# Optimization experiments

Measured on AMD Instinct MI355X. Metric: run time of the kernel, lower is better.

The kernel has to match this reference:

```python
import jax, jax.numpy as jnp
import numpy as np

D = 256          # input_dim (node embedding dim)
ATT_TIMES = 2
ATT_NUM = 2
DIN = D * ATT_NUM  # NTN input dim = 512
F = 16           # feature_map_dim


def setup_inputs() -> dict:
    key = jax.random.key(0)
    ks = jax.random.split(key, 10)
    x1 = jax.random.normal(ks[0], (120000, D), dtype=jnp.float32)
    x2 = jax.random.normal(ks[1], (100000, D), dtype=jnp.float32)
    # attention weight (glorot)
    W0 = jax.random.normal(ks[2], (D, D), dtype=jnp.float32) * (2.0 / (D + D)) ** 0.5
    # NTN params
    V = jax.random.normal(ks[3], (F, 2 * DIN), dtype=jnp.float32) * (2.0 / (F + 2 * DIN)) ** 0.5
    W = jax.random.normal(ks[4], (F, DIN, DIN), dtype=jnp.float32) * (2.0 / (DIN + DIN)) ** 0.5
    b = jax.random.normal(ks[5], (F,), dtype=jnp.float32)
    # projection MLP 16->8->4->2->1, torch Linear weights are (out, in)
    P0 = jax.random.normal(ks[6], (8, 16), dtype=jnp.float32) * (2.0 / (8 + 16)) ** 0.5
    P1 = jax.random.normal(ks[7], (4, 8), dtype=jnp.float32) * (2.0 / (4 + 8)) ** 0.5
    P2 = jax.random.normal(ks[8], (2, 4), dtype=jnp.float32) * (2.0 / (2 + 4)) ** 0.5
    P3 = jax.random.normal(ks[9], (1, 2), dtype=jnp.float32) * (2.0 / (1 + 2)) ** 0.5
    return {"x1": x1, "x2": x2, "W0": W0, "V": V, "W": W, "b": b,
            "P0": P0, "P1": P1, "P2": P2, "P3": P3}


def _attention(x, W0):
    # x: (N, D) -> (1, D*ATT_NUM) graph embedding.
    outs = []
    for _ in range(ATT_NUM):  # 'dot' style: same params each head (eye W), kept for faithfulness
        cur = x
        out = None
        for _ in range(ATT_TIMES):
            temp = jnp.mean(cur, axis=0, keepdims=True)          # (1, D)
            h_avg = jnp.tanh(temp @ W0)                          # att_weight=True
            att = jax.nn.sigmoid(cur @ h_avg.T)                  # (N, 1), W=eye in 'dot' style
            out = att.T @ cur                                    # (1, D)
            cur = cur * att
        outs.append(out)
    return jnp.concatenate(outs, axis=1)                         # (1, DIN)


def _ntn(g1, g2, V, W, b):
    # g1, g2: (1, DIN). Fused bilinear over all F feature maps.
    concat = jnp.concatenate([g1, g2], axis=1)                   # (1, 2*DIN)
    v_term = concat @ V.T                                        # (1, F)
    w_term = jnp.einsum('nd,fde,me->nf', g1, W, g2)              # (1, F)
    return jax.nn.sigmoid(v_term + w_term + b)                   # inneract = sigmoid


def reference(x1, x2, W0, V, W, b, P0, P1, P2, P3):
    g1 = _attention(x1, W0)
    g2 = _attention(x2, W0)
    x = _ntn(g1, g2, V, W, b)                                    # (1, F), branch 'an'
    for P in (P0, P1, P2, P3):                                   # Linear(no bias) + Sigmoid
        x = jax.nn.sigmoid(x @ P.T)
    return x                                                     # (1, 1)
```

## Files before the change

kernel.cpp:

```cpp
#include <hip/hip_runtime.h>
#include <math.h>

#define DD 256
#define REPS 8

#define OFF_SUMREP 0
#define OFF_H1P    4096
#define OFF_S1REP  4608
#define OFF_H2P    8704
#define OFF_OREP   9216
#define OFF_WTREP  13824
#define WS_FLOATS  13952
#define MIRROR_OFF_BYTES 65536

typedef float    f32x4 __attribute__((ext_vector_type(4)));
typedef float    f32x8 __attribute__((ext_vector_type(8)));
typedef _Float16 f16x4 __attribute__((ext_vector_type(4)));
typedef _Float16 f16x8 __attribute__((ext_vector_type(8)));

__device__ __forceinline__ float sigmoidf_(float x) { return 1.0f / (1.0f + __expf(-x)); }

__device__ __forceinline__ f32x8 ld8(const f16x8* p, size_t i) {
    return __builtin_convertvector(p[i], f32x8);
}
__device__ __forceinline__ f32x8 ld8(const f32x8* p, size_t i) { return p[i]; }

__device__ __forceinline__ float dot8(f32x8 a, f32x8 b) {
    f32x8 m = a * b;
    return ((m[0] + m[4]) + (m[1] + m[5])) + ((m[2] + m[6]) + (m[3] + m[7]));
}

__global__ void k_zero(float* __restrict__ ws) {
    int i = blockIdx.x * 256 + threadIdx.x;
    if (i < WS_FLOATS) ws[i] = 0.0f;
}

__device__ __forceinline__ void block_reduce_atomic4(f32x4 acc, int t, float* dst_base) {
    __shared__ f32x4 lds[256];
    lds[t] = acc;
    __syncthreads();
    if (t < 64) {
        f32x4 s = lds[t] + lds[t + 64] + lds[t + 128] + lds[t + 192];
        float* dst = dst_base + t * 4;
        atomicAdd(dst + 0, s.x); atomicAdd(dst + 1, s.y);
        atomicAdd(dst + 2, s.z); atomicAdd(dst + 3, s.w);
    }
}

__device__ __forceinline__ void block_reduce_atomic8(f32x8 acc, int t, float* dst_base) {
    __shared__ f32x8 lds8[256];
    lds8[t] = acc;
    __syncthreads();
    const float* lf = (const float*)lds8;
    float s = 0.f;
#pragma unroll
    for (int slot = 0; slot < 8; slot++) s += lf[slot * 256 + t];
    atomicAdd(dst_base + t, s);
}

template<bool WM>
__global__ void k_mean_t(const f32x4* __restrict__ x1, const f32x4* __restrict__ x2,
                         f16x4* __restrict__ m1, f16x4* __restrict__ m2,
                         int N1, int N2, float* __restrict__ ws) {
    int b = blockIdx.x, t = threadIdx.x;
    int inp = (b < 512) ? 0 : 1;
    int bl = inp ? (b - 512) : b;
    const f32x4* x = inp ? x2 : x1;
    f16x4* mm = inp ? m2 : m1;
    int N = inp ? N2 : N1;
    int col4 = t & 63, rg = t >> 6;
    f32x4 acc = {0.f, 0.f, 0.f, 0.f};
    for (int r = bl * 4 + rg; r < N; r += 2048) {
        size_t i0 = (size_t)r * 64 + col4;
        f32x4 v = __builtin_nontemporal_load(&x[i0]);
        if (WM) mm[i0] = __builtin_convertvector(v, f16x4);
        acc += v;
    }
    block_reduce_atomic4(acc, t, ws + OFF_SUMREP + inp * (REPS * 256) + (bl & (REPS - 1)) * 256);
}

__global__ void k_hpart(const float* __restrict__ W0, float* __restrict__ ws,
                        int srcOff, int dstOff, int N1, int N2) {
    int inp = blockIdx.x >> 4, g = blockIdx.x & 15;
    int t = threadIdx.x;
    __shared__ float temp[16];
    if (t < 16) {
        const float* src = ws + srcOff + inp * (REPS * 256) + g * 16 + t;
        float s = 0.f;
#pragma unroll
        for (int r = 0; r < REPS; r++) s += src[r * 256];
        temp[t] = s * (1.0f / (float)(inp ? N2 : N1));
    }
    __syncthreads();
    float p = 0.f;
#pragma unroll
    for (int j = 0; j < 16; j++) p += temp[j] * W0[(g * 16 + j) * 256 + t];
    atomicAdd(ws + dstOff + inp * 256 + t, p);
}

template<typename T>
__global__ void k_att1_t(const T* __restrict__ b1, const T* __restrict__ b2,
                         int N1, int N2, float* __restrict__ ws) {
    int b = blockIdx.x, t = threadIdx.x;
    int inp = (b < 512) ? 0 : 1;
    int bl = inp ? (b - 512) : b;
    const T* x = inp ? b2 : b1;
    int N = inp ? N2 : N1;
    int lane = t & 63, w = t >> 6;
    int half = lane >> 5, l32 = lane & 31;
    f32x8 h1;
#pragma unroll
    for (int j = 0; j < 8; j++) h1[j] = tanhf(ws[OFF_H1P + inp * 256 + l32 * 8 + j]);
    f32x8 acc = {0.f, 0.f, 0.f, 0.f, 0.f, 0.f, 0.f, 0.f};
    int wid = bl * 4 + w;
    int base = wid * 2;
    for (; base + 1 < N; base += 4096) {
        int row = base + half;
        f32x8 v = ld8(x, (size_t)row * 32 + l32);
        float d = dot8(v, h1);
#pragma unroll
        for (int off = 16; off; off >>= 1) d += __shfl_xor(d, off, 64);
        acc += sigmoidf_(d) * v;
    }
    if (base < N && half == 0) {
        f32x8 v = ld8(x, (size_t)base * 32 + l32);
        float d = dot8(v, h1);
#pragma unroll
        for (int off = 16; off; off >>= 1) d += __shfl_xor(d, off, 64);
        acc += sigmoidf_(d) * v;
    }
    block_reduce_atomic8(acc, t, ws + OFF_S1REP + inp * (REPS * 256) + (bl & (REPS - 1)) * 256);
}

template<typename T>
__global__ void k_att2_t(const T* __restrict__ b1, const T* __restrict__ b2,
                         int N1, int N2, float* __restrict__ ws) {
    int b = blockIdx.x, t = threadIdx.x;
    int inp = (b < 512) ? 0 : 1;
    int bl = inp ? (b - 512) : b;
    const T* x = inp ? b2 : b1;
    int N = inp ? N2 : N1;
    int lane = t & 63, w = t >> 6;
    int half = lane >> 5, l32 = lane & 31;
    f32x8 h1, h2;
#pragma unroll
    for (int j = 0; j < 8; j++) {
        h1[j] = tanhf(ws[OFF_H1P + inp * 256 + l32 * 8 + j]);
        h2[j] = tanhf(ws[OFF_H2P + inp * 256 + l32 * 8 + j]);
    }
    f32x8 acc = {0.f, 0.f, 0.f, 0.f, 0.f, 0.f, 0.f, 0.f};
    int wid = bl * 4 + w;
    int base = wid * 2;
    for (; base + 1 < N; base += 4096) {
        int row = base + half;
        f32x8 v = ld8(x, (size_t)row * 32 + l32);
        float d = dot8(v, h1), e = dot8(v, h2);
#pragma unroll
        for (int off = 16; off; off >>= 1) {
            d += __shfl_xor(d, off, 64); e += __shfl_xor(e, off, 64);
        }
        float a1 = sigmoidf_(d);
        acc += (a1 * sigmoidf_(a1 * e)) * v;
    }
    if (base < N && half == 0) {
        f32x8 v = ld8(x, (size_t)base * 32 + l32);
        float d = dot8(v, h1), e = dot8(v, h2);
#pragma unroll
        for (int off = 16; off; off >>= 1) {
            d += __shfl_xor(d, off, 64); e += __shfl_xor(e, off, 64);
        }
        float a1 = sigmoidf_(d);
        acc += (a1 * sigmoidf_(a1 * e)) * v;
    }
    block_reduce_atomic8(acc, t, ws + OFF_OREP + inp * (REPS * 256) + (bl & (REPS - 1)) * 256);
}

__global__ void __launch_bounds__(256, 4)
k_ntn(const float* __restrict__ W, float* __restrict__ ws) {
    __shared__ __align__(16) float o_l[512];
    int b = blockIdx.x, t = threadIdx.x;
    {
        float s0 = 0.f, s1 = 0.f;
#pragma unroll
        for (int r2 = 0; r2 < REPS; r2++) {
            s0 += ws[OFF_OREP + r2 * 256 + t];
            s1 += ws[OFF_OREP + REPS * 256 + r2 * 256 + t];
        }
        o_l[t] = s0; o_l[256 + t] = s1;
    }
    __syncthreads();
    int lane = t & 63, w = t >> 6;
    f32x4 o2f = ((const f32x4*)(o_l + 256))[lane];
    int g = b * 4 + w;
    const f32x4* W4 = (const f32x4*)W;
    float wt[4];
    int fidx[4];
#pragma unroll
    for (int u = 0; u < 4; u++) {
        int row = g + u * 2048;
        const f32x4* q = W4 + (size_t)row * 128 + lane;
        f32x4 m = (q[0] + q[64]) * o2f;
        float p = (m.x + m.y) + (m.z + m.w);
#pragma unroll
        for (int off = 32; off; off >>= 1) p += __shfl_xor(p, off, 64);
        wt[u] = o_l[row & 255] * p;
        fidx[u] = row >> 9;
    }
    if (lane == 0) {
        float* dst = ws + OFF_WTREP + (b & (REPS - 1)) * 16;
#pragma unroll
        for (int u = 0; u < 4; u++) atomicAdd(dst + fidx[u], wt[u]);
    }
}

__global__ void k_final(const float* __restrict__ V, const float* __restrict__ bb,
                        const float* __restrict__ P0, const float* __restrict__ P1,
                        const float* __restrict__ P2, const float* __restrict__ P3,
                        float* __restrict__ ws, float* __restrict__ out) {
    int t = threadIdx.x;
    __shared__ float o_l[512];
    {
        float s0 = 0.f, s1 = 0.f;
#pragma unroll
        for (int r2 = 0; r2 < REPS; r2++) {
            s0 += ws[OFF_OREP + r2 * 256 + t];
            s1 += ws[OFF_OREP + REPS * 256 + r2 * 256 + t];
        }
        o_l[t] = s0; o_l[256 + t] = s1;
    }
    __syncthreads();
    int f = t >> 4, j = t & 15;
    float p = 0.f;
    for (int k = j; k < 1024; k += 16) {
        float cv = (k < 512) ? o_l[k & 255] : o_l[256 + (k & 255)];
        p += cv * V[f * 1024 + k];
    }
    __shared__ float red[256];
    __shared__ float sv[16];
    red[t] = p;
    __syncthreads();
    if (t < 16) {
        float v = 0.f;
#pragma unroll
        for (int q = 0; q < 16; q++) v += red[t * 16 + q];
        float wt = 0.f;
#pragma unroll
        for (int r = 0; r < REPS; r++) wt += ws[OFF_WTREP + r * 16 + t];
        sv[t] = sigmoidf_(v + wt + bb[t]);
    }
    __syncthreads();
    if (t == 0) {
        float y0[8], y1[4], y2[2];
#pragma unroll
        for (int i = 0; i < 8; i++) {
            float s = 0.f;
            for (int k = 0; k < 16; k++) s += P0[i * 16 + k] * sv[k];
            y0[i] = sigmoidf_(s);
        }
#pragma unroll
        for (int i = 0; i < 4; i++) {
            float s = 0.f;
            for (int k = 0; k < 8; k++) s += P1[i * 8 + k] * y0[k];
            y1[i] = sigmoidf_(s);
        }
#pragma unroll
        for (int i = 0; i < 2; i++) {
            float s = 0.f;
            for (int k = 0; k < 4; k++) s += P2[i * 4 + k] * y1[k];
            y2[i] = sigmoidf_(s);
        }
        out[0] = sigmoidf_(P3[0] * y2[0] + P3[1] * y2[1]);
    }
}

extern "C" void kernel_launch(void* const* d_in, const int* in_sizes, int n_in,
                              void* d_out, int out_size, void* d_ws, size_t ws_size,
                              hipStream_t stream) {
    const float* x1 = (const float*)d_in[0];
    const float* x2 = (const float*)d_in[1];
    const float* W0 = (const float*)d_in[2];
    const float* V  = (const float*)d_in[3];
    const float* W  = (const float*)d_in[4];
    const float* b  = (const float*)d_in[5];
    const float* P0 = (const float*)d_in[6];
    const float* P1 = (const float*)d_in[7];
    const float* P2 = (const float*)d_in[8];
    const float* P3 = (const float*)d_in[9];
    float* ws  = (float*)d_ws;
    float* out = (float*)d_out;
    int N1 = in_sizes[0] / DD;
    int N2 = in_sizes[1] / DD;

    const f32x4* x1v = (const f32x4*)x1;
    const f32x4* x2v = (const f32x4*)x2;
    f16x4* m1 = (f16x4*)((char*)d_ws + MIRROR_OFF_BYTES);
    f16x4* m2 = m1 + (size_t)N1 * 64;
    size_t need = (size_t)MIRROR_OFF_BYTES + ((size_t)N1 + N2) * DD * sizeof(_Float16);
    bool use_mirror = ws_size >= need;

    k_zero <<<55, 256, 0, stream>>>(ws);
    if (use_mirror) {
        k_mean_t<true>  <<<1024, 256, 0, stream>>>(x1v, x2v, m1, m2, N1, N2, ws);
        k_hpart         <<<32,   256, 0, stream>>>(W0, ws, OFF_SUMREP, OFF_H1P, N1, N2);
        k_att1_t<f16x8> <<<1024, 256, 0, stream>>>((const f16x8*)m1, (const f16x8*)m2, N1, N2, ws);
        k_hpart         <<<32,   256, 0, stream>>>(W0, ws, OFF_S1REP, OFF_H2P, N1, N2);
        k_att2_t<f16x8> <<<1024, 256, 0, stream>>>((const f16x8*)m1, (const f16x8*)m2, N1, N2, ws);
    } else {
        k_mean_t<false> <<<1024, 256, 0, stream>>>(x1v, x2v, nullptr, nullptr, N1, N2, ws);
        k_hpart         <<<32,   256, 0, stream>>>(W0, ws, OFF_SUMREP, OFF_H1P, N1, N2);
        k_att1_t<f32x8> <<<1024, 256, 0, stream>>>((const f32x8*)x1, (const f32x8*)x2, N1, N2, ws);
        k_hpart         <<<32,   256, 0, stream>>>(W0, ws, OFF_S1REP, OFF_H2P, N1, N2);
        k_att2_t<f32x8> <<<1024, 256, 0, stream>>>((const f32x8*)x1, (const f32x8*)x2, N1, N2, ws);
    }
    k_ntn  <<<512, 256, 0, stream>>>(W, ws);
    k_final<<<1,   256, 0, stream>>>(V, b, P0, P1, P2, P3, ws, out);
}
```

Before: 381.0 us.

## Replace global atomic reductions with per-block partial stores and deterministic reductions

Each streaming kernel now writes its block partial sums to a dedicated slot instead of atomically adding into replicated accumulators. Small 2-block reduction kernels (k_h, k_redo) then sum the 512 partials per input, and k_final sums the NTN partials in shared memory. This removes the zeroing kernel and global atomic contention. The cost is an extra launch and serial reductions running on only two blocks, plus a larger workspace that pushes the fp16 mirror offset higher.

```diff
diff --git a/kernel.cpp b/kernel.cpp
--- a/kernel.cpp
+++ b/kernel.cpp
@@ -2,16 +2,15 @@
 #include <math.h>
 
 #define DD 256
-#define REPS 8
-
-#define OFF_SUMREP 0
-#define OFF_H1P    4096
-#define OFF_S1REP  4608
-#define OFF_H2P    8704
-#define OFF_OREP   9216
-#define OFF_WTREP  13824
-#define WS_FLOATS  13952
-#define MIRROR_OFF_BYTES 65536
+
+#define OFF_PARTA  0
+#define OFF_PARTB  262144
+#define OFF_PARTO  524288
+#define OFF_H1P    786432
+#define OFF_H2P    786944
+#define OFF_O      787456
+#define OFF_PWT    787968
+#define MIRROR_OFF_BYTES 4194304
 
 typedef float    f32x4 __attribute__((ext_vector_type(4)));
 typedef float    f32x8 __attribute__((ext_vector_type(8)));
@@ -30,24 +29,17 @@
     return ((m[0] + m[4]) + (m[1] + m[5])) + ((m[2] + m[6]) + (m[3] + m[7]));
 }
 
-__global__ void k_zero(float* __restrict__ ws) {
-    int i = blockIdx.x * 256 + threadIdx.x;
-    if (i < WS_FLOATS) ws[i] = 0.0f;
-}
-
-__device__ __forceinline__ void block_reduce_atomic4(f32x4 acc, int t, float* dst_base) {
+__device__ __forceinline__ void block_reduce_store4(f32x4 acc, int t, float* dst) {
     __shared__ f32x4 lds[256];
     lds[t] = acc;
     __syncthreads();
     if (t < 64) {
         f32x4 s = lds[t] + lds[t + 64] + lds[t + 128] + lds[t + 192];
-        float* dst = dst_base + t * 4;
-        atomicAdd(dst + 0, s.x); atomicAdd(dst + 1, s.y);
-        atomicAdd(dst + 2, s.z); atomicAdd(dst + 3, s.w);
-    }
-}
-
-__device__ __forceinline__ void block_reduce_atomic8(f32x8 acc, int t, float* dst_base) {
+        ((f32x4*)dst)[t] = s;
+    }
+}
+
+__device__ __forceinline__ void block_reduce_store8(f32x8 acc, int t, float* dst) {
     __shared__ f32x8 lds8[256];
     lds8[t] = acc;
     __syncthreads();
@@ -55,7 +47,7 @@
     float s = 0.f;
 #pragma unroll
     for (int slot = 0; slot < 8; slot++) s += lf[slot * 256 + t];
-    atomicAdd(dst_base + t, s);
+    dst[t] = s;
 }
 
 template<bool WM>
@@ -76,26 +68,47 @@
         if (WM) mm[i0] = __builtin_convertvector(v, f16x4);
         acc += v;
     }
-    block_reduce_atomic4(acc, t, ws + OFF_SUMREP + inp * (REPS * 256) + (bl & (REPS - 1)) * 256);
-}
-
-__global__ void k_hpart(const float* __restrict__ W0, float* __restrict__ ws,
-                        int srcOff, int dstOff, int N1, int N2) {
-    int inp = blockIdx.x >> 4, g = blockIdx.x & 15;
-    int t = threadIdx.x;
-    __shared__ float temp[16];
-    if (t < 16) {
-        const float* src = ws + srcOff + inp * (REPS * 256) + g * 16 + t;
-        float s = 0.f;
-#pragma unroll
-        for (int r = 0; r < REPS; r++) s += src[r * 256];
-        temp[t] = s * (1.0f / (float)(inp ? N2 : N1));
+    block_reduce_store4(acc, t, ws + OFF_PARTA + ((size_t)inp * 512 + bl) * 256);
+}
+
+__global__ void k_h(const float* __restrict__ W0, float* __restrict__ ws,
+                    int srcOff, int dstOff, int N1, int N2) {
+    int inp = blockIdx.x, t = threadIdx.x;
+    int col = t & 255, q = t >> 8;
+    const float* src = ws + srcOff + (size_t)inp * 512 * 256;
+    float s = 0.f;
+#pragma unroll 4
+    for (int k = q * 128; k < q * 128 + 128; k++) s += src[k * 256 + col];
+    __shared__ float part[4][256];
+    part[q][col] = s;
+    __syncthreads();
+    __shared__ float temp[256];
+    if (t < 256) {
+        float cs = part[0][t] + part[1][t] + part[2][t] + part[3][t];
+        temp[t] = cs * (1.0f / (float)(inp ? N2 : N1));
     }
     __syncthreads();
     float p = 0.f;
-#pragma unroll
-    for (int j = 0; j < 16; j++) p += temp[j] * W0[(g * 16 + j) * 256 + t];
-    atomicAdd(ws + dstOff + inp * 256 + t, p);
+#pragma unroll 4
+    for (int j = q * 64; j < q * 64 + 64; j++) p += temp[j] * W0[j * 256 + col];
+    part[q][col] = p;
+    __syncthreads();
+    if (t < 256)
+        ws[dstOff + inp * 256 + t] = part[0][t] + part[1][t] + part[2][t] + part[3][t];
+}
+
+__global__ void k_redo(float* __restrict__ ws) {
+    int inp = blockIdx.x, t = threadIdx.x;
+    int col = t & 255, q = t >> 8;
+    const float* src = ws + OFF_PARTO + (size_t)inp * 512 * 256;
+    float s = 0.f;
+#pragma unroll 4
+    for (int k = q * 128; k < q * 128 + 128; k++) s += src[k * 256 + col];
+    __shared__ float part[4][256];
+    part[q][col] = s;
+    __syncthreads();
+    if (t < 256)
+        ws[OFF_O + inp * 256 + t] = part[0][t] + part[1][t] + part[2][t] + part[3][t];
 }
 
 template<typename T>
@@ -129,7 +142,7 @@
         for (int off = 16; off; off >>= 1) d += __shfl_xor(d, off, 64);
         acc += sigmoidf_(d) * v;
     }
-    block_reduce_atomic8(acc, t, ws + OFF_S1REP + inp * (REPS * 256) + (bl & (REPS - 1)) * 256);
+    block_reduce_store8(acc, t, ws + OFF_PARTB + ((size_t)inp * 512 + bl) * 256);
 }
 
 template<typename T>
@@ -172,29 +185,21 @@
         float a1 = sigmoidf_(d);
         acc += (a1 * sigmoidf_(a1 * e)) * v;
     }
-    block_reduce_atomic8(acc, t, ws + OFF_OREP + inp * (REPS * 256) + (bl & (REPS - 1)) * 256);
+    block_reduce_store8(acc, t, ws + OFF_PARTO + ((size_t)inp * 512 + bl) * 256);
 }
 
 __global__ void __launch_bounds__(256, 4)
 k_ntn(const float* __restrict__ W, float* __restrict__ ws) {
     __shared__ __align__(16) float o_l[512];
     int b = blockIdx.x, t = threadIdx.x;
-    {
-        float s0 = 0.f, s1 = 0.f;
-#pragma unroll
-        for (int r2 = 0; r2 < REPS; r2++) {
-            s0 += ws[OFF_OREP + r2 * 256 + t];
-            s1 += ws[OFF_OREP + REPS * 256 + r2 * 256 + t];
-        }
-        o_l[t] = s0; o_l[256 + t] = s1;
-    }
+    o_l[t] = ws[OFF_O + t];
+    o_l[256 + t] = ws[OFF_O + 256 + t];
     __syncthreads();
     int lane = t & 63, w = t >> 6;
     f32x4 o2f = ((const f32x4*)(o_l + 256))[lane];
     int g = b * 4 + w;
     const f32x4* W4 = (const f32x4*)W;
     float wt[4];
-    int fidx[4];
 #pragma unroll
     for (int u = 0; u < 4; u++) {
         int row = g + u * 2048;
@@ -204,12 +209,10 @@
 #pragma unroll
         for (int off = 32; off; off >>= 1) p += __shfl_xor(p, off, 64);
         wt[u] = o_l[row & 255] * p;
-        fidx[u] = row >> 9;
     }
     if (lane == 0) {
-        float* dst = ws + OFF_WTREP + (b & (REPS - 1)) * 16;
-#pragma unroll
-        for (int u = 0; u < 4; u++) atomicAdd(dst + fidx[u], wt[u]);
+#pragma unroll
+        for (int u = 0; u < 4; u++) ws[OFF_PWT + b * 16 + w * 4 + u] = wt[u];
     }
 }
 
@@ -219,16 +222,16 @@
                         float* __restrict__ ws, float* __restrict__ out) {
     int t = threadIdx.x;
     __shared__ float o_l[512];
-    {
-        float s0 = 0.f, s1 = 0.f;
-#pragma unroll
-        for (int r2 = 0; r2 < REPS; r2++) {
-            s0 += ws[OFF_OREP + r2 * 256 + t];
-            s1 += ws[OFF_OREP + REPS * 256 + r2 * 256 + t];
-        }
-        o_l[t] = s0; o_l[256 + t] = s1;
-    }
-    __syncthreads();
+    o_l[t] = ws[OFF_O + t];
+    o_l[256 + t] = ws[OFF_O + 256 + t];
+    __shared__ float wtl[16];
+    if (t < 16) wtl[t] = 0.f;
+    __syncthreads();
+    for (int i = t; i < 8192; i += 256) {
+        int b = i >> 4, w = (i >> 2) & 3, u = i & 3;
+        int f = (b * 4 + w + u * 2048) >> 9;
+        atomicAdd(&wtl[f], ws[OFF_PWT + i]);
+    }
     int f = t >> 4, j = t & 15;
     float p = 0.f;
     for (int k = j; k < 1024; k += 16) {
@@ -243,10 +246,7 @@
         float v = 0.f;
 #pragma unroll
         for (int q = 0; q < 16; q++) v += red[t * 16 + q];
-        float wt = 0.f;
-#pragma unroll
-        for (int r = 0; r < REPS; r++) wt += ws[OFF_WTREP + r * 16 + t];
-        sv[t] = sigmoidf_(v + wt + bb[t]);
+        sv[t] = sigmoidf_(v + wtl[t] + bb[t]);
     }
     __syncthreads();
     if (t == 0) {
@@ -298,20 +298,20 @@
     size_t need = (size_t)MIRROR_OFF_BYTES + ((size_t)N1 + N2) * DD * sizeof(_Float16);
     bool use_mirror = ws_size >= need;
 
-    k_zero <<<55, 256, 0, stream>>>(ws);
     if (use_mirror) {
         k_mean_t<true>  <<<1024, 256, 0, stream>>>(x1v, x2v, m1, m2, N1, N2, ws);
-        k_hpart         <<<32,   256, 0, stream>>>(W0, ws, OFF_SUMREP, OFF_H1P, N1, N2);
+        k_h             <<<2,   1024, 0, stream>>>(W0, ws, OFF_PARTA, OFF_H1P, N1, N2);
         k_att1_t<f16x8> <<<1024, 256, 0, stream>>>((const f16x8*)m1, (const f16x8*)m2, N1, N2, ws);
-        k_hpart         <<<32,   256, 0, stream>>>(W0, ws, OFF_S1REP, OFF_H2P, N1, N2);
+        k_h             <<<2,   1024, 0, stream>>>(W0, ws, OFF_PARTB, OFF_H2P, N1, N2);
         k_att2_t<f16x8> <<<1024, 256, 0, stream>>>((const f16x8*)m1, (const f16x8*)m2, N1, N2, ws);
     } else {
         k_mean_t<false> <<<1024, 256, 0, stream>>>(x1v, x2v, nullptr, nullptr, N1, N2, ws);
-        k_hpart         <<<32,   256, 0, stream>>>(W0, ws, OFF_SUMREP, OFF_H1P, N1, N2);
+        k_h             <<<2,   1024, 0, stream>>>(W0, ws, OFF_PARTA, OFF_H1P, N1, N2);
         k_att1_t<f32x8> <<<1024, 256, 0, stream>>>((const f32x8*)x1, (const f32x8*)x2, N1, N2, ws);
-        k_hpart         <<<32,   256, 0, stream>>>(W0, ws, OFF_S1REP, OFF_H2P, N1, N2);
+        k_h             <<<2,   1024, 0, stream>>>(W0, ws, OFF_PARTB, OFF_H2P, N1, N2);
         k_att2_t<f32x8> <<<1024, 256, 0, stream>>>((const f32x8*)x1, (const f32x8*)x2, N1, N2, ws);
     }
+    k_redo <<<2,  1024, 0, stream>>>(ws);
     k_ntn  <<<512, 256, 0, stream>>>(W, ws);
     k_final<<<1,   256, 0, stream>>>(V, b, P0, P1, P2, P3, ws, out);
 }
```

New measurement: 388.2 us. No clear change (+1.9%).
